# Optimization experiments

Measured on AMD Instinct MI355X. Metric: run time of the kernel, lower is better.

Reference implementation:

```python
import jax, jax.numpy as jnp
import numpy as np

N_HEAD, D_HEAD, D_MODEL = 16, 64, 1024
QLEN, MEMLEN, BSZ = 1024, 1024, 2
KLEN = QLEN + MEMLEN  # rlen == klen
LN_EPS = 1e-5
NEG = -1e30


def _rel_shift(x):
    # x: [qlen, rlen, bsz, n_head] -> Transformer-XL relative shift
    q, r, b, n = x.shape
    zp = jnp.zeros((q, 1, b, n), x.dtype)
    xp = jnp.concatenate([zp, x], axis=1).reshape(r + 1, q, b, n)
    return xp[1:].reshape(q, r, b, n)


def _layer_norm(x, gamma, beta):
    mu = jnp.mean(x, axis=-1, keepdims=True)
    var = jnp.mean((x - mu) ** 2, axis=-1, keepdims=True)
    return (x - mu) * jax.lax.rsqrt(var + LN_EPS) * gamma + beta


def setup_inputs() -> dict:
    key = jax.random.key(0)
    ks = jax.random.split(key, 8)
    w = jax.random.normal(ks[0], (QLEN, BSZ, D_MODEL), jnp.float32)
    r = jax.random.normal(ks[1], (KLEN, D_MODEL), jnp.float32)
    r_w_bias = jax.random.normal(ks[2], (N_HEAD, D_HEAD), jnp.float32) * 0.02
    r_r_bias = jax.random.normal(ks[3], (N_HEAD, D_HEAD), jnp.float32) * 0.02
    mems = jax.random.normal(ks[4], (MEMLEN, BSZ, D_MODEL), jnp.float32)
    W_qkv = jax.random.normal(ks[5], (D_MODEL, 3 * N_HEAD * D_HEAD), jnp.float32) * 0.02
    W_r = jax.random.normal(ks[6], (D_MODEL, N_HEAD * D_HEAD), jnp.float32) * 0.02
    W_o = jax.random.normal(ks[7], (N_HEAD * D_HEAD, D_MODEL), jnp.float32) * 0.02
    ln_gamma = jnp.ones((D_MODEL,), jnp.float32)
    ln_beta = jnp.zeros((D_MODEL,), jnp.float32)
    # causal mask with memory: key j visible to query i iff j <= i + MEMLEN (True = keep)
    attn_mask = jnp.arange(KLEN)[None, :] <= (jnp.arange(QLEN)[:, None] + MEMLEN)
    return {"w": w, "r": r, "r_w_bias": r_w_bias, "r_r_bias": r_r_bias,
            "mems": mems, "attn_mask": attn_mask, "W_qkv": W_qkv, "W_r": W_r,
            "W_o": W_o, "ln_gamma": ln_gamma, "ln_beta": ln_beta}


def reference(w, r, r_w_bias, r_r_bias, mems, attn_mask, W_qkv, W_r, W_o, ln_gamma, ln_beta):
    qlen, bsz = w.shape[0], w.shape[1]
    scale = 1.0 / (D_HEAD ** 0.5)
    cat = jnp.concatenate([mems, w], axis=0)            # [klen, b, d_model]
    klen = cat.shape[0]
    w_heads = cat @ W_qkv                                # [klen, b, 3*H*D]
    r_head_k = (r @ W_r).reshape(-1, N_HEAD, D_HEAD)     # [rlen, H, D]
    w_head_q, w_head_k, w_head_v = jnp.split(w_heads, 3, axis=-1)
    w_head_q = w_head_q[-qlen:].reshape(qlen, bsz, N_HEAD, D_HEAD)
    w_head_k = w_head_k.reshape(klen, bsz, N_HEAD, D_HEAD)
    w_head_v = w_head_v.reshape(klen, bsz, N_HEAD, D_HEAD)
    AC = jnp.einsum('ibnd,jbnd->ijbn', w_head_q + r_w_bias, w_head_k)
    BD = jnp.einsum('ibnd,jnd->ijbn', w_head_q + r_r_bias, r_head_k)
    BD = _rel_shift(BD)
    attn_score = (AC + BD) * scale                       # [q, k, b, n]
    attn_score = jnp.where(attn_mask[:, :, None, None], attn_score, NEG)
    attn_prob = jax.nn.softmax(attn_score, axis=1)
    attn_vec = jnp.einsum('ijbn,jbnd->ibnd', attn_prob, w_head_v)
    attn_vec = attn_vec.reshape(qlen, bsz, N_HEAD * D_HEAD)
    attn_out = attn_vec @ W_o                            # [q, b, d_model]
    return _layer_norm(w + attn_out, ln_gamma, ln_beta)
```

## Files before the change

### kernel.cpp

```cpp
#include <hip/hip_runtime.h>
#include <hip/hip_bf16.h>

#define NHEAD 16
#define DHEAD 64
#define DMODEL 1024
#define QLEN 1024
#define MEMLEN 1024
#define BSZ 2
#define KLEN 2048
#define LN_EPS 1e-5f

typedef __hip_bfloat16 bf16;
typedef __attribute__((ext_vector_type(8))) short short8;
typedef __attribute__((ext_vector_type(4))) float f32x4;

__device__ __forceinline__ float b2f(bf16 x) { return __bfloat162float(x); }
__device__ __forceinline__ bf16 f2b(float x) { return __float2bfloat16(x); }
__device__ __forceinline__ short f2bs(float f) {
    bf16 h = __float2bfloat16(f);
    return *reinterpret_cast<short*>(&h);
}
__device__ __forceinline__ float s2f(short s) {
    bf16 h = *reinterpret_cast<bf16*>(&s);
    return __bfloat162float(h);
}

#define MFMA16(a, b, c) __builtin_amdgcn_mfma_f32_16x16x32_bf16(a, b, c, 0, 0, 0)

#define AS1 __attribute__((address_space(1)))
#define AS3 __attribute__((address_space(3)))
__device__ __forceinline__ void gld16(const bf16* g, bf16* l) {
    __builtin_amdgcn_global_load_lds((const AS1 void*)(uintptr_t)g,
                                     (AS3 void*)(uint32_t)(uintptr_t)l, 16, 0, 0);
}

__global__ __launch_bounds__(256)
void prep(const float* __restrict__ mems, const float* __restrict__ w,
          const float* __restrict__ r, const float* __restrict__ Wqkv,
          const float* __restrict__ Wr, const float* __restrict__ Wo,
          bf16* __restrict__ Abf, bf16* __restrict__ rbf,
          bf16* __restrict__ Wqkvt, bf16* __restrict__ Wrt,
          bf16* __restrict__ Wot) {
    __shared__ bf16 T[64][65];
    const int id = blockIdx.x;
    const int t = threadIdx.x;
    if (id < 6144) {
        const float* src;
        bf16* dst;
        int off;
        if (id < 2048)      { src = mems; dst = Abf;                       off = id; }
        else if (id < 4096) { src = w;    dst = Abf + (size_t)2048 * 1024; off = id - 2048; }
        else                { src = r;    dst = rbf;                       off = id - 4096; }
        int i = off * 256 + t;
        const float4 v = reinterpret_cast<const float4*>(src)[i];
        bf16 o[4] = {f2b(v.x), f2b(v.y), f2b(v.z), f2b(v.w)};
        reinterpret_cast<ulong1*>(dst)[i] = *reinterpret_cast<ulong1*>(o);
        return;
    }
    int tid2 = id - 6144;
    const float* in;
    bf16* out;
    int N, tn, tile;
    if (tid2 < 768)       { in = Wqkv; out = Wqkvt; N = 3072; tn = 48; tile = tid2; }
    else if (tid2 < 1024) { in = Wr;   out = Wrt;   N = 1024; tn = 16; tile = tid2 - 768; }
    else                  { in = Wo;   out = Wot;   N = 1024; tn = 16; tile = tid2 - 1024; }
    const int K = 1024;
    const int n0 = (tile % tn) * 64, k0 = (tile / tn) * 64;
    #pragma unroll
    for (int e = 0; e < 16; e++) {
        int flat = e * 256 + t;
        int kl = flat >> 6, nl = flat & 63;
        T[kl][nl] = f2b(in[(size_t)(k0 + kl) * N + n0 + nl]);
    }
    __syncthreads();
    #pragma unroll
    for (int e = 0; e < 16; e++) {
        int flat = e * 256 + t;
        int nl = flat >> 6, kl = flat & 63;
        out[(size_t)(n0 + nl) * K + k0 + kl] = T[kl][nl];
    }
}

__global__ __launch_bounds__(256)
void gemm_mfma(const bf16* __restrict__ A, const bf16* __restrict__ Bt,
               const bf16* __restrict__ A2, const bf16* __restrict__ B2,
               int M, int N, int K, int mode,
               const float* __restrict__ rwb, const float* __restrict__ rrb,
               bf16* __restrict__ Qw, bf16* __restrict__ Qr,
               bf16* __restrict__ Kb, bf16* __restrict__ Vt,
               bf16* __restrict__ Cb, float* __restrict__ Cf) {
    const int bm = blockIdx.x * 128, bn = blockIdx.y * 128;
    int sub = 0;
    const bf16* Ap = A;
    const bf16* Bp = Bt;
    if (mode == 0 && bm < 2048 && bn < 1024) { sub = 1; Ap = A2; Bp = B2; }
    __shared__ bf16 As[128 * 32];
    __shared__ bf16 Bs[128 * 32];
    const int t = threadIdx.x;
    const int w = t >> 6, lane = t & 63, quad = lane >> 4, l16 = lane & 15;
    const int wm = (w >> 1) * 64, wn = (w & 1) * 64;
    const int lrow = lane >> 2, lcol = (lane & 3) * 8;

    f32x4 acc[4][4];
    #pragma unroll
    for (int mt = 0; mt < 4; mt++)
        #pragma unroll
        for (int nt = 0; nt < 4; nt++) acc[mt][nt] = (f32x4){0.f, 0.f, 0.f, 0.f};

    for (int k0 = 0; k0 < K; k0 += 32) {
        #pragma unroll
        for (int e = 0; e < 2; e++) {
            int ch = w + 4 * e;
            int row = ch * 16 + lrow;
            gld16(Ap + (size_t)(bm + row) * K + k0 + lcol, As + ch * 512);
            gld16(Bp + (size_t)(bn + row) * K + k0 + lcol, Bs + ch * 512);
        }
        __syncthreads();
        short8 af[4], bfr[4];
        #pragma unroll
        for (int mt = 0; mt < 4; mt++)
            af[mt] = *reinterpret_cast<short8*>(&As[(wm + 16 * mt + l16) * 32 + quad * 8]);
        #pragma unroll
        for (int nt = 0; nt < 4; nt++)
            bfr[nt] = *reinterpret_cast<short8*>(&Bs[(wn + 16 * nt + l16) * 32 + quad * 8]);
        #pragma unroll
        for (int mt = 0; mt < 4; mt++)
            #pragma unroll
            for (int nt = 0; nt < 4; nt++)
                acc[mt][nt] = MFMA16(af[mt], bfr[nt], acc[mt][nt]);
        __syncthreads();
    }

    #pragma unroll
    for (int mt = 0; mt < 4; mt++)
        #pragma unroll
        for (int nt = 0; nt < 4; nt++)
            #pragma unroll
            for (int r = 0; r < 4; r++) {
                int m = bm + wm + 16 * mt + quad * 4 + r;
                int c = bn + wn + 16 * nt + l16;
                float v = acc[mt][nt][r];
                if (sub) {
                    Cb[(size_t)m * 1024 + c] = f2b(v);
                } else if (mode == 0) {
                    int seg = c >> 10, cc = c & 1023;
                    if (seg == 0) {
                        if (m >= 2048) {
                            size_t o = (size_t)(m - 2048) * 1024 + cc;
                            Qw[o] = f2b(v + rwb[cc]);
                            Qr[o] = f2b(v + rrb[cc]);
                        }
                    } else if (seg == 1) {
                        Kb[(size_t)m * 1024 + cc] = f2b(v);
                    } else {
                        Vt[((size_t)cc * 2 + (m & 1)) * 2048 + (m >> 1)] = f2b(v);
                    }
                } else {
                    Cf[(size_t)m * N + c] = v;
                }
            }
}

__global__ __launch_bounds__(256, 3)
void attn_mfma(const bf16* __restrict__ Qw, const bf16* __restrict__ Qr,
               const bf16* __restrict__ Kb, const bf16* __restrict__ Vt,
               const bf16* __restrict__ Rk, float* __restrict__ O0g,
               float* __restrict__ O1g, float2* __restrict__ ML) {
    const int id = blockIdx.x;
    const int xcd = id & 7, local = id >> 3;
    const int pidx = local & 3;
    const int couple = (local >> 2) & 7;
    const int chunk = local >> 5;
    const int pair = xcd * 4 + pidx;
    const int b = pair & 1, n = pair >> 1;
    const int TA = couple + 17;
    const int t_beg = (chunk == 0) ? 0 : (chunk == 1) ? 17 : 33;
    const int t_end = (chunk == 0) ? 17 : (chunk == 1) ? 33 : 49;

    int segs[2][4];
    int nseg = 0;
    {
        int aend = min(t_end, TA);
        if (t_beg < aend) {
            segs[nseg][0] = couple; segs[nseg][1] = t_beg;
            segs[nseg][2] = aend;   segs[nseg][3] = (t_beg == 0) ? 0 : 1;
            nseg++;
        }
        int bbeg = max(t_beg, TA);
        if (bbeg < t_end) {
            segs[nseg][0] = 15 - couple; segs[nseg][1] = bbeg - TA;
            segs[nseg][2] = t_end - TA;  segs[nseg][3] = (bbeg == TA) ? 0 : 1;
            nseg++;
        }
    }

    const int tid = threadIdx.x;
    const int w = tid >> 6, lane = tid & 63;
    const int quad = lane >> 4, l16 = lane & 15;
    const int ln8 = lane >> 3;
    const int cs = (lane & 7) ^ (ln8 & 7);
    const int q0 = (quad ^ (l16 & 7)) * 8;
    const int q1 = q0 ^ 32;
    const int rbl = 48 - 16 * w;

    __shared__ bf16 Ks[2][64 * 64];
    __shared__ bf16 Rs[3][64 * 64];
    __shared__ short WP_s[4][16 * 82];
    short* WP = WP_s[w];

    const int koff = b * 1024 + n * 64 + cs * 8;
    const int rcol = n * 64 + cs * 8;
    const size_t vrow0 = ((size_t)(n * 64 + l16) * 2 + b) * 2048 + quad * 8;

    for (int sg = 0; sg < nseg; sg++) {
        const int i0 = segs[sg][0], jb = segs[sg][1], je = segs[sg][2], slot = segs[sg][3];
        const int I0 = i0 * 64;
        const int qbase = I0 + 16 * w;
        const int RB = 960 - I0;

        auto stageK = [&](int tt) {
            const int J0t = tt * 64;
            bf16* kd = Ks[tt & 1];
            #pragma unroll
            for (int e = 0; e < 2; e++) {
                int ch = w + 4 * e;
                int krow = min(J0t + ch * 8 + ln8, 2047);
                gld16(Kb + (size_t)krow * 2048 + koff, kd + ch * 512);
            }
        };
        auto stageR = [&](int u) {
            bf16* rd = Rs[u % 3];
            #pragma unroll
            for (int e = 0; e < 2; e++) {
                int ch = w + 4 * e;
                int rrow = min(RB + u * 64 + ch * 8 + ln8, 2047);
                gld16(Rk + (size_t)rrow * 1024 + rcol, rd + ch * 512);
            }
        };

        short8 aqw[2], aqr[2];
        {
            const bf16* qp = Qw + ((size_t)(qbase + l16) * 2 + b) * 1024 + n * 64 + quad * 8;
            aqw[0] = *reinterpret_cast<const short8*>(qp);
            aqw[1] = *reinterpret_cast<const short8*>(qp + 32);
            const bf16* qp2 = Qr + ((size_t)(qbase + l16) * 2 + b) * 1024 + n * 64 + quad * 8;
            aqr[0] = *reinterpret_cast<const short8*>(qp2);
            aqr[1] = *reinterpret_cast<const short8*>(qp2 + 32);
        }

        f32x4 O[4];
        #pragma unroll
        for (int d = 0; d < 4; d++) O[d] = (f32x4){0.f, 0.f, 0.f, 0.f};
        float m_run = -1e30f;
        float pl[4] = {0.f, 0.f, 0.f, 0.f};

        if (sg) {
            asm volatile("s_waitcnt vmcnt(0)" ::: "memory");
            __builtin_amdgcn_s_barrier();
        }
        stageK(jb); stageR(jb); stageR(jb + 1);

        for (int j = jb; j < je; j++) {
            const int J0 = j * 64;

            asm volatile("s_waitcnt vmcnt(0)" ::: "memory");
            __builtin_amdgcn_s_barrier();

            short8 vf0[4], vf1[4];
            #pragma unroll
            for (int ds = 0; ds < 4; ds++) {
                const bf16* vp = Vt + (vrow0 + (size_t)ds * 65536 + J0);
                vf0[ds] = *reinterpret_cast<const short8*>(vp);
                vf1[ds] = *reinterpret_cast<const short8*>(vp + 32);
            }
            stageK(j + 1);
            stageR(j + 2);

            const bf16* K_ = Ks[j & 1];
            const bf16* R0 = Rs[j % 3];
            const bf16* R1 = Rs[(j + 1) % 3];

            #pragma unroll
            for (int s = 0; s < 5; s++) {
                int rb2 = rbl + 16 * s;
                const bf16* Rb = (rb2 & 64) ? R1 : R0;
                int rh = (rb2 & 63) + l16;
                short8 b0 = *reinterpret_cast<const short8*>(&Rb[rh * 64 + q0]);
                short8 b1 = *reinterpret_cast<const short8*>(&Rb[rh * 64 + q1]);
                f32x4 acc = (f32x4){0.f, 0.f, 0.f, 0.f};
                __builtin_amdgcn_s_setprio(1);
                acc = MFMA16(aqr[0], b0, acc);
                acc = MFMA16(aqr[1], b1, acc);
                __builtin_amdgcn_s_setprio(0);
                #pragma unroll
                for (int r = 0; r < 4; r++)
                    WP[(quad * 4 + r) * 82 + 16 * s + l16] = f2bs(acc[r]);
            }

            float sv[4][4];
            #pragma unroll
            for (int n16 = 0; n16 < 4; n16++) {
                int kr = 16 * n16 + l16;
                short8 k0 = *reinterpret_cast<const short8*>(&K_[kr * 64 + q0]);
                short8 k1 = *reinterpret_cast<const short8*>(&K_[kr * 64 + q1]);
                f32x4 acc = (f32x4){0.f, 0.f, 0.f, 0.f};
                __builtin_amdgcn_s_setprio(1);
                acc = MFMA16(aqw[0], k0, acc);
                acc = MFMA16(aqw[1], k1, acc);
                __builtin_amdgcn_s_setprio(0);
                #pragma unroll
                for (int r = 0; r < 4; r++) {
                    int row = quad * 4 + r, col = 16 * n16 + l16;
                    float s = (acc[r] + s2f(WP[row * 82 + col - row + 15])) * 0.125f;
                    if (J0 + col > qbase + row + MEMLEN) s = -1e30f;
                    sv[n16][r] = s;
                }
            }

            float mx = sv[0][0];
            #pragma unroll
            for (int n16 = 0; n16 < 4; n16++)
                #pragma unroll
                for (int r = 0; r < 4; r++) mx = fmaxf(mx, sv[n16][r]);
            #pragma unroll
            for (int msk = 1; msk < 16; msk <<= 1) mx = fmaxf(mx, __shfl_xor(mx, msk));
            if (mx > m_run + 8.f) {
                const float alpha = __expf(m_run - mx);
                m_run = mx;
                #pragma unroll
                for (int r = 0; r < 4; r++) pl[r] *= alpha;
                #pragma unroll
                for (int d = 0; d < 4; d++)
                    #pragma unroll
                    for (int r = 0; r < 4; r++) O[d][r] *= alpha;
            }
            #pragma unroll
            for (int n16 = 0; n16 < 4; n16++)
                #pragma unroll
                for (int r = 0; r < 4; r++) sv[n16][r] = __expf(sv[n16][r] - m_run);
            #pragma unroll
            for (int r = 0; r < 4; r++)
                pl[r] += sv[0][r] + sv[1][r] + sv[2][r] + sv[3][r];

            #pragma unroll
            for (int n16 = 0; n16 < 4; n16++)
                #pragma unroll
                for (int r = 0; r < 4; r++)
                    WP[(quad * 4 + r) * 72 + 16 * n16 + l16] = f2bs(sv[n16][r]);
            short8 ap0 = *reinterpret_cast<short8*>(&WP[l16 * 72 + quad * 8]);
            short8 ap1 = *reinterpret_cast<short8*>(&WP[l16 * 72 + 32 + quad * 8]);

            __builtin_amdgcn_s_setprio(1);
            #pragma unroll
            for (int ds = 0; ds < 4; ds++) {
                O[ds] = MFMA16(ap0, vf0[ds], O[ds]);
                O[ds] = MFMA16(ap1, vf1[ds], O[ds]);
            }
            __builtin_amdgcn_s_setprio(0);
        }

        float lr[4];
        #pragma unroll
        for (int r = 0; r < 4; r++) {
            float s = pl[r];
            #pragma unroll
            for (int msk = 1; msk < 16; msk <<= 1) s += __shfl_xor(s, msk);
            lr[r] = s;
        }
        if (l16 == 0) {
            #pragma unroll
            for (int r = 0; r < 4; r++) {
                int q = qbase + quad * 4 + r;
                ML[(size_t)slot * 32768 + (q * 2 + b) * 16 + n] =
                    make_float2(m_run, lr[r]);
            }
        }
        float* Od = slot ? O1g : O0g;
        #pragma unroll
        for (int ds = 0; ds < 4; ds++)
            #pragma unroll
            for (int r = 0; r < 4; r++) {
                int q = qbase + quad * 4 + r;
                Od[((size_t)q * 2 + b) * 1024 + n * 64 + 16 * ds + l16] = O[ds][r];
            }
    }
}

__global__ __launch_bounds__(256)
void attn_combine(const float* __restrict__ O0, const float* __restrict__ O1,
                  const float2* __restrict__ ML, bf16* __restrict__ AVbf) {
    const int row = blockIdx.x;
    const int t = threadIdx.x;
    const int n = t >> 4;
    const int i0 = row >> 7;
    const float2 a0 = ML[row * 16 + n];
    const f32x4 p0 = reinterpret_cast<const f32x4*>(O0)[row * 256 + t];
    short o[4];
    if (i0 != 0) {
        const float2 a1 = ML[32768 + row * 16 + n];
        const float m = fmaxf(a0.x, a1.x);
        const float e0 = __expf(a0.x - m);
        const float e1 = __expf(a1.x - m);
        const float inv = 1.f / (a0.y * e0 + a1.y * e1);
        const f32x4 p1 = reinterpret_cast<const f32x4*>(O1)[row * 256 + t];
        #pragma unroll
        for (int jj = 0; jj < 4; jj++)
            o[jj] = f2bs((p0[jj] * e0 + p1[jj] * e1) * inv);
    } else {
        const float inv = 1.f / a0.y;
        #pragma unroll
        for (int jj = 0; jj < 4; jj++) o[jj] = f2bs(p0[jj] * inv);
    }
    reinterpret_cast<ulong1*>(AVbf)[row * 256 + t] = *reinterpret_cast<ulong1*>(o);
}

__global__ __launch_bounds__(256)
void ln_res(const float* __restrict__ ao, const float* __restrict__ w,
            const float* __restrict__ gamma, const float* __restrict__ beta,
            float* __restrict__ out) {
    const int m = blockIdx.x;
    const int t = threadIdx.x;
    __shared__ float red[256];
    float x[4];
    #pragma unroll
    for (int e = 0; e < 4; e++) {
        int c = e * 256 + t;
        x[e] = ao[(size_t)m * DMODEL + c] + w[(size_t)m * DMODEL + c];
    }
    float s = x[0] + x[1] + x[2] + x[3];
    red[t] = s;
    __syncthreads();
    #pragma unroll
    for (int off = 128; off; off >>= 1) {
        if (t < off) red[t] += red[t + off];
        __syncthreads();
    }
    const float mu = red[0] * (1.f / 1024.f);
    __syncthreads();
    float s2 = 0.f;
    #pragma unroll
    for (int e = 0; e < 4; e++) { float dx = x[e] - mu; s2 += dx * dx; }
    red[t] = s2;
    __syncthreads();
    #pragma unroll
    for (int off = 128; off; off >>= 1) {
        if (t < off) red[t] += red[t + off];
        __syncthreads();
    }
    const float rstd = rsqrtf(red[0] * (1.f / 1024.f) + LN_EPS);
    #pragma unroll
    for (int e = 0; e < 4; e++) {
        int c = e * 256 + t;
        out[(size_t)m * DMODEL + c] = (x[e] - mu) * rstd * gamma[c] + beta[c];
    }
}

extern "C" void kernel_launch(void* const* d_in, const int* in_sizes, int n_in,
                              void* d_out, int out_size, void* d_ws, size_t ws_size,
                              hipStream_t stream) {
    const float* w        = (const float*)d_in[0];
    const float* r        = (const float*)d_in[1];
    const float* r_w_bias = (const float*)d_in[2];
    const float* r_r_bias = (const float*)d_in[3];
    const float* mems     = (const float*)d_in[4];
    const float* W_qkv    = (const float*)d_in[6];
    const float* W_r      = (const float*)d_in[7];
    const float* W_o      = (const float*)d_in[8];
    const float* gamma    = (const float*)d_in[9];
    const float* beta     = (const float*)d_in[10];
    float* out = (float*)d_out;

    bf16* Abf    = (bf16*)d_ws;
    bf16* Wqkvt  = Abf   + (size_t)4096 * 1024;
    bf16* Wrt    = Wqkvt + (size_t)3072 * 1024;
    bf16* Wot    = Wrt   + (size_t)1024 * 1024;
    bf16* rbf    = Wot   + (size_t)1024 * 1024;
    bf16* Qw     = rbf   + (size_t)2048 * 1024;
    bf16* Qr     = Qw    + (size_t)2048 * 1024;
    bf16* Kb     = Qr    + (size_t)2048 * 1024;
    bf16* Vt     = Kb    + (size_t)4096 * 1024;
    bf16* Rk     = Vt    + (size_t)2048 * 2048;
    bf16* AVbf   = Rk    + (size_t)2048 * 1024;
    float* attn_out = (float*)Abf;
    float* Opart0   = (float*)Abf;
    float* Opart1   = (float*)Wqkvt;
    float2* ML      = (float2*)rbf;

    dim3 b256(256);
    prep<<<dim3(7424), b256, 0, stream>>>(mems, w, r, W_qkv, W_r, W_o,
                                          Abf, rbf, Wqkvt, Wrt, Wot);
    gemm_mfma<<<dim3(32, 24), b256, 0, stream>>>(
        Abf, Wqkvt, rbf, Wrt, 4096, 3072, 1024, 0, r_w_bias, r_r_bias,
        Qw, Qr, Kb, Vt, Rk, nullptr);
    attn_mfma<<<dim3(768), b256, 0, stream>>>(Qw, Qr, Kb, Vt, Rk,
                                              Opart0, Opart1, ML);
    attn_combine<<<dim3(2048), b256, 0, stream>>>(Opart0, Opart1, ML, AVbf);
    gemm_mfma<<<dim3(16, 8), b256, 0, stream>>>(
        AVbf, Wot, nullptr, nullptr, 2048, 1024, 1024, 2, nullptr, nullptr,
        nullptr, nullptr, nullptr, nullptr, nullptr, attn_out);
    ln_res<<<dim3(QLEN * BSZ), b256, 0, stream>>>(attn_out, w, gamma, beta, out);
}
```

Before: 262.3 us.

## Stage V through LDS with K, fold log2e scale into Q, mask only diagonal tile

Q projections are pre-scaled by log2(e)/sqrt(d) so softmax uses native exp2 with no per-score multiply. Masking is applied only on the last (diagonal) key tile instead of every tile. V is now loaded into LDS alongside K in the current iteration, with a partial vmcnt wait overlapping the loads with the BD computation. This replaces the per-lane direct global V loads and the K double buffer. The trade-off is a single-buffered K/V tile, an extra barrier per iteration, and K/V load latency exposed within the iteration rather than prefetched.

```diff
diff --git a/kernel.cpp b/kernel.cpp
--- a/kernel.cpp
+++ b/kernel.cpp
@@ -23,6 +23,11 @@
 __device__ __forceinline__ float s2f(short s) {
     bf16 h = *reinterpret_cast<bf16*>(&s);
     return __bfloat162float(h);
+}
+__device__ __forceinline__ float fexp2(float x) {
+    float y;
+    asm("v_exp_f32 %0, %1" : "=v"(y) : "v"(x));
+    return y;
 }
 
 #define MFMA16(a, b, c) __builtin_amdgcn_mfma_f32_16x16x32_bf16(a, b, c, 0, 0, 0)
@@ -131,6 +136,7 @@
         __syncthreads();
     }
 
+    const float QSC = 0.18033688f;
     #pragma unroll
     for (int mt = 0; mt < 4; mt++)
         #pragma unroll
@@ -147,8 +153,8 @@
                     if (seg == 0) {
                         if (m >= 2048) {
                             size_t o = (size_t)(m - 2048) * 1024 + cc;
-                            Qw[o] = f2b(v + rwb[cc]);
-                            Qr[o] = f2b(v + rrb[cc]);
+                            Qw[o] = f2b((v + rwb[cc]) * QSC);
+                            Qr[o] = f2b((v + rrb[cc]) * QSC);
                         }
                     } else if (seg == 1) {
                         Kb[(size_t)m * 1024 + cc] = f2b(v);
@@ -203,29 +209,30 @@
     const int q1 = q0 ^ 32;
     const int rbl = 48 - 16 * w;
 
-    __shared__ bf16 Ks[2][64 * 64];
+    __shared__ bf16 Ks[64 * 64];
+    __shared__ bf16 Vs[64 * 64];
     __shared__ bf16 Rs[3][64 * 64];
     __shared__ short WP_s[4][16 * 82];
     short* WP = WP_s[w];
 
     const int koff = b * 1024 + n * 64 + cs * 8;
+    const size_t voff = (size_t)n * 262144 + b * 2048 + cs * 8;
     const int rcol = n * 64 + cs * 8;
-    const size_t vrow0 = ((size_t)(n * 64 + l16) * 2 + b) * 2048 + quad * 8;
 
     for (int sg = 0; sg < nseg; sg++) {
         const int i0 = segs[sg][0], jb = segs[sg][1], je = segs[sg][2], slot = segs[sg][3];
         const int I0 = i0 * 64;
         const int qbase = I0 + 16 * w;
         const int RB = 960 - I0;
-
-        auto stageK = [&](int tt) {
+        const int jlast = i0 + 16;
+
+        auto stageKV = [&](int tt) {
             const int J0t = tt * 64;
-            bf16* kd = Ks[tt & 1];
             #pragma unroll
             for (int e = 0; e < 2; e++) {
                 int ch = w + 4 * e;
-                int krow = min(J0t + ch * 8 + ln8, 2047);
-                gld16(Kb + (size_t)krow * 2048 + koff, kd + ch * 512);
+                gld16(Vt + (size_t)(ch * 8 + ln8) * 4096 + voff + J0t, Vs + ch * 512);
+                gld16(Kb + (size_t)(J0t + ch * 8 + ln8) * 2048 + koff, Ks + ch * 512);
             }
         };
         auto stageR = [&](int u) {
@@ -258,7 +265,7 @@
             asm volatile("s_waitcnt vmcnt(0)" ::: "memory");
             __builtin_amdgcn_s_barrier();
         }
-        stageK(jb); stageR(jb); stageR(jb + 1);
+        stageR(jb); stageR(jb + 1);
 
         for (int j = jb; j < je; j++) {
             const int J0 = j * 64;
@@ -266,17 +273,9 @@
             asm volatile("s_waitcnt vmcnt(0)" ::: "memory");
             __builtin_amdgcn_s_barrier();
 
-            short8 vf0[4], vf1[4];
-            #pragma unroll
-            for (int ds = 0; ds < 4; ds++) {
-                const bf16* vp = Vt + (vrow0 + (size_t)ds * 65536 + J0);
-                vf0[ds] = *reinterpret_cast<const short8*>(vp);
-                vf1[ds] = *reinterpret_cast<const short8*>(vp + 32);
-            }
-            stageK(j + 1);
+            stageKV(j);
             stageR(j + 2);
 
-            const bf16* K_ = Ks[j & 1];
             const bf16* R0 = Rs[j % 3];
             const bf16* R1 = Rs[(j + 1) % 3];
 
@@ -297,12 +296,15 @@
                     WP[(quad * 4 + r) * 82 + 16 * s + l16] = f2bs(acc[r]);
             }
 
+            asm volatile("s_waitcnt vmcnt(2)" ::: "memory");
+            __builtin_amdgcn_s_barrier();
+
             float sv[4][4];
             #pragma unroll
             for (int n16 = 0; n16 < 4; n16++) {
                 int kr = 16 * n16 + l16;
-                short8 k0 = *reinterpret_cast<const short8*>(&K_[kr * 64 + q0]);
-                short8 k1 = *reinterpret_cast<const short8*>(&K_[kr * 64 + q1]);
+                short8 k0 = *reinterpret_cast<const short8*>(&Ks[kr * 64 + q0]);
+                short8 k1 = *reinterpret_cast<const short8*>(&Ks[kr * 64 + q1]);
                 f32x4 acc = (f32x4){0.f, 0.f, 0.f, 0.f};
                 __builtin_amdgcn_s_setprio(1);
                 acc = MFMA16(aqw[0], k0, acc);
@@ -311,11 +313,18 @@
                 #pragma unroll
                 for (int r = 0; r < 4; r++) {
                     int row = quad * 4 + r, col = 16 * n16 + l16;
-                    float s = (acc[r] + s2f(WP[row * 82 + col - row + 15])) * 0.125f;
-                    if (J0 + col > qbase + row + MEMLEN) s = -1e30f;
-                    sv[n16][r] = s;
+                    sv[n16][r] = acc[r] + s2f(WP[row * 82 + col - row + 15]);
                 }
             }
+            if (j == jlast) {
+                #pragma unroll
+                for (int n16 = 0; n16 < 4; n16++)
+                    #pragma unroll
+                    for (int r = 0; r < 4; r++) {
+                        int row = quad * 4 + r, col = 16 * n16 + l16;
+                        if (J0 + col > qbase + row + MEMLEN) sv[n16][r] = -1e30f;
+                    }
+            }
 
             float mx = sv[0][0];
             #pragma unroll
@@ -324,8 +333,8 @@
                 for (int r = 0; r < 4; r++) mx = fmaxf(mx, sv[n16][r]);
             #pragma unroll
             for (int msk = 1; msk < 16; msk <<= 1) mx = fmaxf(mx, __shfl_xor(mx, msk));
-            if (mx > m_run + 8.f) {
-                const float alpha = __expf(m_run - mx);
+            if (mx > m_run + 11.5f) {
+                const float alpha = fexp2(m_run - mx);
                 m_run = mx;
                 #pragma unroll
                 for (int r = 0; r < 4; r++) pl[r] *= alpha;
@@ -337,7 +346,7 @@
             #pragma unroll
             for (int n16 = 0; n16 < 4; n16++)
                 #pragma unroll
-                for (int r = 0; r < 4; r++) sv[n16][r] = __expf(sv[n16][r] - m_run);
+                for (int r = 0; r < 4; r++) sv[n16][r] = fexp2(sv[n16][r] - m_run);
             #pragma unroll
             for (int r = 0; r < 4; r++)
                 pl[r] += sv[0][r] + sv[1][r] + sv[2][r] + sv[3][r];
@@ -353,8 +362,11 @@
             __builtin_amdgcn_s_setprio(1);
             #pragma unroll
             for (int ds = 0; ds < 4; ds++) {
-                O[ds] = MFMA16(ap0, vf0[ds], O[ds]);
-                O[ds] = MFMA16(ap1, vf1[ds], O[ds]);
+                int dr = 16 * ds + l16;
+                short8 v0 = *reinterpret_cast<const short8*>(&Vs[dr * 64 + q0]);
+                short8 v1 = *reinterpret_cast<const short8*>(&Vs[dr * 64 + q1]);
+                O[ds] = MFMA16(ap0, v0, O[ds]);
+                O[ds] = MFMA16(ap1, v1, O[ds]);
             }
             __builtin_amdgcn_s_setprio(0);
         }
@@ -399,8 +411,8 @@
     if (i0 != 0) {
         const float2 a1 = ML[32768 + row * 16 + n];
         const float m = fmaxf(a0.x, a1.x);
-        const float e0 = __expf(a0.x - m);
-        const float e1 = __expf(a1.x - m);
+        const float e0 = fexp2(a0.x - m);
+        const float e1 = fexp2(a1.x - m);
         const float inv = 1.f / (a0.y * e0 + a1.y * e1);
         const f32x4 p1 = reinterpret_cast<const f32x4*>(O1)[row * 256 + t];
         #pragma unroll
```

After: 248.2 us. -5.4%, faster.
